# Kernel tuning notes

Measured on AMD Instinct MI355X. Metric: run time of the kernel, lower is better.

The kernel has to match this reference:

```python
import jax, jax.numpy as jnp
import numpy as np

N_NODES = 50000
N_EDGES = 800000
IN_CH = 128
OUT_CH = 64


def setup_inputs() -> dict:
    key = jax.random.key(0)
    ks = jax.random.split(key, 8)
    cat = IN_CH + OUT_CH
    scale = 1.0 / np.sqrt(cat)
    return {
        "x": jax.random.normal(ks[0], (N_NODES, IN_CH), dtype=jnp.float32),
        "edge_index": jax.random.randint(ks[1], (2, N_EDGES), 0, N_NODES, dtype=jnp.int64),
        "edge_weight": jax.random.uniform(ks[2], (N_EDGES,), dtype=jnp.float32),
        "hidden_state": jax.random.normal(ks[3], (N_NODES, OUT_CH), dtype=jnp.float32),
        "W_z": jax.random.normal(ks[4], (cat, OUT_CH), dtype=jnp.float32) * scale,
        "b_z": jnp.zeros((OUT_CH,), dtype=jnp.float32),
        "W_r": jax.random.normal(ks[5], (cat, OUT_CH), dtype=jnp.float32) * scale,
        "b_r": jnp.zeros((OUT_CH,), dtype=jnp.float32),
        "W_h": jax.random.normal(ks[6], (cat, OUT_CH), dtype=jnp.float32) * scale,
        "b_h": jnp.zeros((OUT_CH,), dtype=jnp.float32),
    }


def _gcn_norm(row, col, w, num_nodes):
    # PyG GCNConv normalization with self-loops (fill_value=1):
    # norm_e = deg[row]^-1/2 * w_e * deg[col]^-1/2 over loop-augmented edges
    loops = jnp.arange(num_nodes, dtype=row.dtype)
    row = jnp.concatenate([row, loops])
    col = jnp.concatenate([col, loops])
    w = jnp.concatenate([w, jnp.ones((num_nodes,), dtype=w.dtype)])
    deg = jax.ops.segment_sum(w, col, num_segments=num_nodes)
    dinv = jnp.where(deg > 0, jax.lax.rsqrt(deg), 0.0)
    norm = dinv[row] * w * dinv[col]
    return row, col, norm


def _gcn_conv(x_cat, W, b, row, col, norm, num_nodes):
    h = x_cat @ W                                   # (N, out)
    msg = h[row] * norm[:, None]                    # (E+N, out) gather + scale
    out = jax.ops.segment_sum(msg, col, num_segments=num_nodes)
    return out + b


def reference(x, edge_index, edge_weight, hidden_state,
              W_z, b_z, W_r, b_r, W_h, b_h):
    n = x.shape[0]
    row, col, norm = _gcn_norm(edge_index[0], edge_index[1], edge_weight, n)
    xh = jnp.concatenate([x, hidden_state], axis=1)
    z = jax.nn.sigmoid(_gcn_conv(xh, W_z, b_z, row, col, norm, n))
    r = jax.nn.sigmoid(_gcn_conv(xh, W_r, b_r, row, col, norm, n))
    xrh = jnp.concatenate([x, r * hidden_state], axis=1)
    h_cand = jnp.tanh(_gcn_conv(xrh, W_h, b_h, row, col, norm, n))
    return z * hidden_state + (1.0 - z) * h_cand
```

## Files before the change

### kernel.cpp

```cpp
#include <hip/hip_runtime.h>
#include <hip/hip_bf16.h>
#include <cstdint>
#include <cstddef>

#define IN_CH   128
#define OUT_CH  64
#define CAT_CH  192

typedef short bf16x8 __attribute__((ext_vector_type(8)));
typedef float f32x4  __attribute__((ext_vector_type(4)));
typedef float f32x2  __attribute__((ext_vector_type(2)));
typedef unsigned long long u64;
typedef unsigned int u32;

__device__ __forceinline__ float sigmoidf_(float x) { return 1.f / (1.f + __expf(-x)); }

__device__ __forceinline__ unsigned short f2bf(float f) {
    u32 u = __float_as_uint(f);
    u32 r = (u + 0x7fffu + ((u >> 16) & 1u)) >> 16;
    return (unsigned short)r;
}
__device__ __forceinline__ float bflo(u32 v) { return __uint_as_float(v << 16); }
__device__ __forceinline__ float bfhi(u32 v) { return __uint_as_float(v & 0xffff0000u); }

__device__ __forceinline__ unsigned char f2e4m3(float f) {
    u32 p = __builtin_amdgcn_cvt_pk_fp8_f32(f, f, 0, false);
    return (unsigned char)p;
}
template <bool HI>
__device__ __forceinline__ f32x2 fp8pk(u32 v) {
    return __builtin_amdgcn_cvt_pk_f32_fp8((int)v, HI);
}

__global__ void detect_kernel(const unsigned int* __restrict__ ei, int* __restrict__ flag) {
    unsigned int v = ei[(threadIdx.x << 1) + 1];
    unsigned long long b = __ballot(v != 0u);
    if (threadIdx.x == 0) *flag = (b != 0ull) ? 1 : 0;
}

__device__ __forceinline__ int load_col(const void* ei, int i, int E, int f) {
    return f ? ((const int*)ei)[E + i] : (int)((const long long*)ei)[E + i];
}
__device__ __forceinline__ int load_row(const void* ei, int i, int E, int f) {
    return f ? ((const int*)ei)[i] : (int)((const long long*)ei)[i];
}

__global__ void hist2_kernel(const void* __restrict__ ei, const float* __restrict__ w,
                             u64* __restrict__ packed, u32* __restrict__ rank,
                             const int* __restrict__ flag, int E) {
    int i0 = (blockIdx.x * blockDim.x + threadIdx.x) * 4;
    if (i0 >= E) return;
    int f = *flag;
    u32 rk[4];
#pragma unroll
    for (int k = 0; k < 4; k++) {
        int i = i0 + k;
        if (i < E) {
            int c = load_col(ei, i, E, f);
            u32 wq = __float2uint_rn(w[i] * 1048576.0f);
            u64 old = atomicAdd(&packed[c], (1ull << 32) | (u64)wq);
            rk[k] = (u32)(old >> 32);
        }
    }
#pragma unroll
    for (int k = 0; k < 4; k++)
        if (i0 + k < E) rank[i0 + k] = rk[k];
}

__global__ __launch_bounds__(256) void scan1_kernel(const u64* __restrict__ packed,
                                                    float* __restrict__ dinv,
                                                    int* __restrict__ starts,
                                                    int* __restrict__ bsum, int n) {
    __shared__ int s[256];
    int i = blockIdx.x * 256 + threadIdx.x;
    int v = 0;
    if (i < n) {
        u64 p = packed[i];
        float wsum = (float)(u32)(p & 0xffffffffull) * (1.0f / 1048576.0f);
        dinv[i] = rsqrtf(1.0f + wsum);
        v = (int)(p >> 32);
    }
    s[threadIdx.x] = v;
    __syncthreads();
#pragma unroll
    for (int d = 1; d < 256; d <<= 1) {
        int t = (threadIdx.x >= d) ? s[threadIdx.x - d] : 0;
        __syncthreads();
        s[threadIdx.x] += t;
        __syncthreads();
    }
    if (i < n) starts[i] = s[threadIdx.x] - v;
    if (threadIdx.x == 255) bsum[blockIdx.x] = s[255];
}

__global__ __launch_bounds__(256) void scan2_kernel(int* __restrict__ bsum, int nb) {
    __shared__ int s[256];
    int t = threadIdx.x;
    int v = (t < nb) ? bsum[t] : 0;
    s[t] = v;
    __syncthreads();
#pragma unroll
    for (int d = 1; d < 256; d <<= 1) {
        int u = (t >= d) ? s[t - d] : 0;
        __syncthreads();
        s[t] += u;
        __syncthreads();
    }
    if (t < nb) bsum[t] = s[t] - v;
}

__global__ void scan3_kernel(int* __restrict__ starts, const int* __restrict__ boff,
                             int n, int E) {
    int i = blockIdx.x * blockDim.x + threadIdx.x;
    if (i == 0) starts[n] = E;
    if (i < n) starts[i] += boff[blockIdx.x];
}

__global__ void scatter2_kernel(const void* __restrict__ ei, const float* __restrict__ w,
                                const float* __restrict__ dinv, const int* __restrict__ starts,
                                const u32* __restrict__ rank, u64* __restrict__ pairs,
                                const int* __restrict__ flag, int E) {
    int i0 = (blockIdx.x * blockDim.x + threadIdx.x) * 4;
    if (i0 >= E) return;
    int f = *flag;
    int r[4], c[4];
#pragma unroll
    for (int k = 0; k < 4; k++) {
        int i = i0 + k;
        if (i < E) { r[k] = load_row(ei, i, E, f); c[k] = load_col(ei, i, E, f); }
    }
#pragma unroll
    for (int k = 0; k < 4; k++) {
        int i = i0 + k;
        if (i < E) {
            float nm = dinv[r[k]] * w[i] * dinv[c[k]];
            int pos = starts[c[k]] + (int)rank[i];
            pairs[pos] = ((u64)__float_as_uint(nm) << 32) | (u32)(r[k] << 7);
        }
    }
}

__global__ void cvt_kernel(const float* __restrict__ x, const float* __restrict__ hidden,
                           unsigned short* __restrict__ xb, unsigned short* __restrict__ hb,
                           int nx, int nh) {
    int i4 = (blockIdx.x * blockDim.x + threadIdx.x) * 4;
    if (i4 < nx) {
        float4 v = *(const float4*)&x[i4];
        ushort4 o = { f2bf(v.x), f2bf(v.y), f2bf(v.z), f2bf(v.w) };
        *(ushort4*)&xb[i4] = o;
    } else {
        int j = i4 - nx;
        if (j < nh) {
            float4 v = *(const float4*)&hidden[j];
            ushort4 o = { f2bf(v.x), f2bf(v.y), f2bf(v.z), f2bf(v.w) };
            *(ushort4*)&hb[j] = o;
        }
    }
}

__global__ void packW_kernel(const float* __restrict__ Wz, const float* __restrict__ Wr,
                             const float* __restrict__ Wh,
                             unsigned short* __restrict__ Bzrt, unsigned short* __restrict__ Wht) {
    int i = blockIdx.x * blockDim.x + threadIdx.x;
    if (i >= 192 * CAT_CH) return;
    int col = i / CAT_CH, k = i % CAT_CH;
    if (col < 128) {
        float v = (col < 64) ? Wz[k * 64 + col] : Wr[k * 64 + (col - 64)];
        Bzrt[col * CAT_CH + k] = f2bf(v);
    } else {
        Wht[(col - 128) * CAT_CH + k] = f2bf(Wh[k * 64 + (col - 128)]);
    }
}

template <int TN, bool FP8OUT>
__global__ __launch_bounds__(256) void gemm_bf16_kernel(
    const unsigned short* __restrict__ A0, int a0w,
    const unsigned short* __restrict__ A1, int a1w,
    const unsigned short* __restrict__ Bt,
    void* __restrict__ Cout, int nrows)
{
    __shared__ unsigned short As[128][48];
    __shared__ unsigned short Bs[TN][200];

    const int t = threadIdx.x, lane = t & 63, wave = t >> 6;
    const int rowBase = blockIdx.x * 128;

    for (int idx = t * 8; idx < TN * CAT_CH; idx += 256 * 8) {
        int col = idx / CAT_CH, k = idx % CAT_CH;
        *(int4*)&Bs[col][k] = *(const int4*)&Bt[idx];
    }

    f32x4 acc[2][TN / 16];
#pragma unroll
    for (int rf = 0; rf < 2; rf++)
#pragma unroll
        for (int cf = 0; cf < TN / 16; cf++) acc[rf][cf] = (f32x4){0.f, 0.f, 0.f, 0.f};

    const int srow = t >> 1, half = t & 1;
    int arow = rowBase + srow;
    if (arow >= nrows) arow = nrows - 1;

    for (int k0 = 0; k0 < CAT_CH; k0 += 32) {
        __syncthreads();
        {
            const unsigned short* src = (k0 < a0w)
                ? A0 + (size_t)arow * a0w + k0
                : A1 + (size_t)arow * a1w + (k0 - a0w);
            *(int4*)&As[srow][half * 16] = *(const int4*)(src + half * 16);
            *(int4*)&As[srow][half * 16 + 8] = *(const int4*)(src + half * 16 + 8);
        }
        __syncthreads();

        const int rbase = wave * 32;
        const int koff = (lane >> 4) * 8;
        bf16x8 a0 = *(const bf16x8*)&As[rbase + (lane & 15)][koff];
        bf16x8 a1 = *(const bf16x8*)&As[rbase + 16 + (lane & 15)][koff];
#pragma unroll
        for (int cf = 0; cf < TN / 16; cf++) {
            bf16x8 b = *(const bf16x8*)&Bs[cf * 16 + (lane & 15)][k0 + koff];
            acc[0][cf] = __builtin_amdgcn_mfma_f32_16x16x32_bf16(a0, b, acc[0][cf], 0, 0, 0);
            acc[1][cf] = __builtin_amdgcn_mfma_f32_16x16x32_bf16(a1, b, acc[1][cf], 0, 0, 0);
        }
    }

#pragma unroll
    for (int rf = 0; rf < 2; rf++)
#pragma unroll
        for (int cf = 0; cf < TN / 16; cf++) {
            int row0 = rowBase + wave * 32 + rf * 16 + (lane >> 4) * 4;
            int col  = cf * 16 + (lane & 15);
#pragma unroll
            for (int r = 0; r < 4; r++) {
                int row = row0 + r;
                if (row < nrows) {
                    if (FP8OUT)
                        ((unsigned char*)Cout)[(size_t)row * TN + col] = f2e4m3(acc[rf][cf][r]);
                    else
                        ((unsigned short*)Cout)[(size_t)row * TN + col] = f2bf(acc[rf][cf][r]);
                }
            }
        }
}

__global__ __launch_bounds__(256) void spmm_zr_kernel(
    const unsigned char* __restrict__ H8, const u64* __restrict__ pairs,
    const int* __restrict__ starts, const float* __restrict__ dinv,
    const float* __restrict__ hidden, const float* __restrict__ bz,
    const float* __restrict__ br, float* __restrict__ Z,
    unsigned short* __restrict__ RHb, int N)
{
    int node = (blockIdx.x * 256 + threadIdx.x) >> 6;
    if (node >= N) return;
    const int lane = threadIdx.x & 63;
    const int sub = lane & 31, half = lane >> 5;
    int s = starts[node], e = starts[node + 1];
    float d = dinv[node], d2 = d * d;

    float a0 = 0.f, a1 = 0.f, a2 = 0.f, a3 = 0.f;
    if (half == 0) {
        u32 sv = *(const u32*)&H8[(size_t)node * 128 + sub * 4];
        f32x2 s01 = fp8pk<false>(sv), s23 = fp8pk<true>(sv);
        a0 = s01.x * d2; a1 = s01.y * d2; a2 = s23.x * d2; a3 = s23.y * d2;
    }

    int j = s;
    int full = s + ((e - s) & ~15);
    for (; j < full; j += 16) {
        u32 hv[8]; float nm[8];
#pragma unroll
        for (int k = 0; k < 8; k++) {
            u64 p = pairs[j + k * 2 + half];
            nm[k] = __uint_as_float((u32)(p >> 32));
            hv[k] = *(const u32*)&H8[(size_t)(u32)p + sub * 4];
        }
#pragma unroll
        for (int k = 0; k < 8; k++) {
            f32x2 h01 = fp8pk<false>(hv[k]), h23 = fp8pk<true>(hv[k]);
            a0 = fmaf(h01.x, nm[k], a0); a1 = fmaf(h01.y, nm[k], a1);
            a2 = fmaf(h23.x, nm[k], a2); a3 = fmaf(h23.y, nm[k], a3);
        }
    }
    if (j < e) {
        u32 hv[8]; float nm[8];
#pragma unroll
        for (int k = 0; k < 8; k++) {
            int jj = j + k * 2 + half;
            u64 p = pairs[(jj < e) ? jj : (e - 1)];
            nm[k] = (jj < e) ? __uint_as_float((u32)(p >> 32)) : 0.f;
            hv[k] = *(const u32*)&H8[(size_t)(u32)p + sub * 4];
        }
#pragma unroll
        for (int k = 0; k < 8; k++) {
            f32x2 h01 = fp8pk<false>(hv[k]), h23 = fp8pk<true>(hv[k]);
            a0 = fmaf(h01.x, nm[k], a0); a1 = fmaf(h01.y, nm[k], a1);
            a2 = fmaf(h23.x, nm[k], a2); a3 = fmaf(h23.y, nm[k], a3);
        }
    }

    a0 += __shfl_xor(a0, 32, 64);
    a1 += __shfl_xor(a1, 32, 64);
    a2 += __shfl_xor(a2, 32, 64);
    a3 += __shfl_xor(a3, 32, 64);

    if (half == 0) {
        if (sub < 16) {
            int c = sub * 4;
            float4 b4 = *(const float4*)&bz[c];
            float4 o = { sigmoidf_(a0 + b4.x), sigmoidf_(a1 + b4.y),
                         sigmoidf_(a2 + b4.z), sigmoidf_(a3 + b4.w) };
            *(float4*)&Z[(size_t)node * 64 + c] = o;
        } else {
            int c = (sub - 16) * 4;
            float4 b4 = *(const float4*)&br[c];
            float4 hid = *(const float4*)&hidden[(size_t)node * 64 + c];
            float r0 = sigmoidf_(a0 + b4.x) * hid.x;
            float r1 = sigmoidf_(a1 + b4.y) * hid.y;
            float r2 = sigmoidf_(a2 + b4.z) * hid.z;
            float r3 = sigmoidf_(a3 + b4.w) * hid.w;
            ushort4 o = { f2bf(r0), f2bf(r1), f2bf(r2), f2bf(r3) };
            *(ushort4*)&RHb[(size_t)node * 64 + c] = o;
        }
    }
}

__global__ __launch_bounds__(256) void spmm_h_kernel(
    const unsigned short* __restrict__ H, const u64* __restrict__ pairs,
    const int* __restrict__ starts, const float* __restrict__ dinv,
    const float* __restrict__ hidden, const float* __restrict__ bh,
    const float* __restrict__ Z, float* __restrict__ out, int N)
{
    int node = (blockIdx.x * 256 + threadIdx.x) >> 6;
    if (node >= N) return;
    const int lane = threadIdx.x & 63;
    const int sub = lane & 31, half = lane >> 5;
    const unsigned char* Hb = (const unsigned char*)H;
    int s = starts[node], e = starts[node + 1];
    float d = dinv[node], d2 = d * d;

    float ax = 0.f, ay = 0.f;
    if (half == 0) {
        u32 sv = *(const u32*)&Hb[(size_t)node * 128 + sub * 4];
        ax = bflo(sv) * d2; ay = bfhi(sv) * d2;
    }

    int j = s;
    int full = s + ((e - s) & ~15);
    for (; j < full; j += 16) {
        u32 hv[8]; float nm[8];
#pragma unroll
        for (int k = 0; k < 8; k++) {
            u64 p = pairs[j + k * 2 + half];
            nm[k] = __uint_as_float((u32)(p >> 32));
            hv[k] = *(const u32*)&Hb[(size_t)(u32)p + sub * 4];
        }
#pragma unroll
        for (int k = 0; k < 8; k++) {
            ax = fmaf(bflo(hv[k]), nm[k], ax);
            ay = fmaf(bfhi(hv[k]), nm[k], ay);
        }
    }
    if (j < e) {
        u32 hv[8]; float nm[8];
#pragma unroll
        for (int k = 0; k < 8; k++) {
            int jj = j + k * 2 + half;
            u64 p = pairs[(jj < e) ? jj : (e - 1)];
            nm[k] = (jj < e) ? __uint_as_float((u32)(p >> 32)) : 0.f;
            hv[k] = *(const u32*)&Hb[(size_t)(u32)p + sub * 4];
        }
#pragma unroll
        for (int k = 0; k < 8; k++) {
            ax = fmaf(bflo(hv[k]), nm[k], ax);
            ay = fmaf(bfhi(hv[k]), nm[k], ay);
        }
    }

    ax += __shfl_xor(ax, 32, 64);
    ay += __shfl_xor(ay, 32, 64);

    if (half == 0) {
        int c = sub * 2;
        size_t idx = (size_t)node * 64 + c;
        float2 hid = *(const float2*)&hidden[idx];
        float2 z   = *(const float2*)&Z[idx];
        float hc0 = tanhf(ax + bh[c]);
        float hc1 = tanhf(ay + bh[c + 1]);
        float2 o = { z.x * hid.x + (1.f - z.x) * hc0,
                     z.y * hid.y + (1.f - z.y) * hc1 };
        *(float2*)&out[idx] = o;
    }
}

extern "C" void kernel_launch(void* const* d_in, const int* in_sizes, int n_in,
                              void* d_out, int out_size, void* d_ws, size_t ws_size,
                              hipStream_t stream) {
    const float* x      = (const float*)d_in[0];
    const void*  eidx   = d_in[1];
    const float* ew     = (const float*)d_in[2];
    const float* hidden = (const float*)d_in[3];
    const float* Wz     = (const float*)d_in[4];
    const float* bz     = (const float*)d_in[5];
    const float* Wr     = (const float*)d_in[6];
    const float* br     = (const float*)d_in[7];
    const float* Wh     = (const float*)d_in[8];
    const float* bh     = (const float*)d_in[9];
    float* out = (float*)d_out;

    const int E = in_sizes[2];
    const int N = in_sizes[3] / OUT_CH;

    char* base = (char*)d_ws;
    size_t off = 0;
    auto carve = [&](size_t bytes) -> char* {
        char* p = base + off;
        off = (off + bytes + 255) & ~(size_t)255;
        return p;
    };
    u64*   packed = (u64*)  carve((size_t)N * 8);
    u32*   rank   = (u32*)  carve((size_t)E * 4);
    float* dinv   = (float*)carve((size_t)N * 4);
    int*   starts = (int*)  carve((size_t)(N + 1) * 4);
    int*   bsum   = (int*)  carve(256 * 4);
    u64*   pairs  = (u64*)  carve((size_t)E * 8);
    unsigned short* xb   = (unsigned short*)carve((size_t)N * 128 * 2);
    unsigned short* hb   = (unsigned short*)carve((size_t)N * 64 * 2);
    unsigned char*  Hzr8 = (unsigned char*)carve((size_t)N * 128);
    unsigned short* RHb  = (unsigned short*)carve((size_t)N * 64 * 2);
    unsigned short* Hhb  = (unsigned short*)carve((size_t)N * 64 * 2);
    float* Z = (float*)carve((size_t)N * 64 * 4);
    unsigned short* Bzrt = (unsigned short*)carve((size_t)128 * CAT_CH * 2);
    unsigned short* Wht  = (unsigned short*)carve((size_t)64 * CAT_CH * 2);
    int* flag = (int*)carve(4);
    if (off > ws_size) return;

    const int B256 = 256;
    const int gE4 = (E + 1023) / 1024;
    const int gN = (N + B256 - 1) / B256;
    const int gM = (N + 127) / 128;
    const int gW = (N + 3) / 4;

    hipLaunchKernelGGL(detect_kernel, dim3(1), dim3(64), 0, stream,
                       (const unsigned int*)eidx, flag);

    (void)hipMemsetAsync(packed, 0, (size_t)N * 8, stream);
    hipLaunchKernelGGL(hist2_kernel, dim3(gE4), dim3(B256), 0, stream,
                       eidx, ew, packed, rank, flag, E);

    hipLaunchKernelGGL(scan1_kernel, dim3(gN), dim3(B256), 0, stream,
                       packed, dinv, starts, bsum, N);
    hipLaunchKernelGGL(scan2_kernel, dim3(1), dim3(B256), 0, stream, bsum, gN);
    hipLaunchKernelGGL(scan3_kernel, dim3(gN), dim3(B256), 0, stream, starts, bsum, N, E);

    hipLaunchKernelGGL(scatter2_kernel, dim3(gE4), dim3(B256), 0, stream,
                       eidx, ew, dinv, starts, rank, pairs, flag, E);

    hipLaunchKernelGGL(cvt_kernel, dim3((N * CAT_CH / 4 + 255) / 256), dim3(B256), 0, stream,
                       x, hidden, xb, hb, N * 128, N * 64);
    hipLaunchKernelGGL(packW_kernel, dim3((192 * CAT_CH + 255) / 256), dim3(B256), 0, stream,
                       Wz, Wr, Wh, Bzrt, Wht);

    hipLaunchKernelGGL((gemm_bf16_kernel<128, true>), dim3(gM), dim3(B256), 0, stream,
                       xb, 128, hb, 64, Bzrt, (void*)Hzr8, N);

    hipLaunchKernelGGL(spmm_zr_kernel, dim3(gW), dim3(B256), 0, stream,
                       Hzr8, pairs, starts, dinv, hidden, bz, br, Z, RHb, N);

    hipLaunchKernelGGL((gemm_bf16_kernel<64, false>), dim3(gM), dim3(B256), 0, stream,
                       xb, 128, RHb, 64, Wht, (void*)Hhb, N);

    hipLaunchKernelGGL(spmm_h_kernel, dim3(gW), dim3(B256), 0, stream,
                       Hhb, pairs, starts, dinv, hidden, bh, Z, out, N);
}
```

Measured before the change: 178.7 us.

## Shard degree histogram atomics across eight copies to cut contention

The per-node packed count/weight histogram is replicated into 8 shards, selected by block index, so that concurrent 64-bit atomics spread over more addresses. The scan kernel sums the shards per node and writes per-shard offsets, and the scatter kernel adds the shard offset to the rank, which now carries the shard id in its top bits. The histogram kernel also processes 2 edges per thread instead of 4. This costs a larger memset, 8x more histogram reads in the scan, and an extra gathered offset read per edge in the scatter.

```diff
diff --git a/kernel.cpp b/kernel.cpp
--- a/kernel.cpp
+++ b/kernel.cpp
@@ -46,39 +46,49 @@
 }
 
 __global__ void hist2_kernel(const void* __restrict__ ei, const float* __restrict__ w,
-                             u64* __restrict__ packed, u32* __restrict__ rank,
-                             const int* __restrict__ flag, int E) {
-    int i0 = (blockIdx.x * blockDim.x + threadIdx.x) * 4;
+                             u64* __restrict__ packed8, u32* __restrict__ rank,
+                             const int* __restrict__ flag, int E, int N) {
+    int i0 = (blockIdx.x * blockDim.x + threadIdx.x) * 2;
     if (i0 >= E) return;
+    const u32 shard = blockIdx.x & 7;
+    u64* __restrict__ shp = packed8 + (size_t)shard * N;
     int f = *flag;
-    u32 rk[4];
-#pragma unroll
-    for (int k = 0; k < 4; k++) {
+    u32 rk[2];
+#pragma unroll
+    for (int k = 0; k < 2; k++) {
         int i = i0 + k;
         if (i < E) {
             int c = load_col(ei, i, E, f);
             u32 wq = __float2uint_rn(w[i] * 1048576.0f);
-            u64 old = atomicAdd(&packed[c], (1ull << 32) | (u64)wq);
-            rk[k] = (u32)(old >> 32);
-        }
-    }
-#pragma unroll
-    for (int k = 0; k < 4; k++)
+            u64 old = atomicAdd(&shp[c], (1ull << 32) | (u64)wq);
+            rk[k] = (shard << 28) | (u32)(old >> 32);
+        }
+    }
+#pragma unroll
+    for (int k = 0; k < 2; k++)
         if (i0 + k < E) rank[i0 + k] = rk[k];
 }
 
-__global__ __launch_bounds__(256) void scan1_kernel(const u64* __restrict__ packed,
+__global__ __launch_bounds__(256) void scan1_kernel(const u64* __restrict__ packed8,
                                                     float* __restrict__ dinv,
+                                                    u32* __restrict__ shoff,
                                                     int* __restrict__ starts,
                                                     int* __restrict__ bsum, int n) {
     __shared__ int s[256];
     int i = blockIdx.x * 256 + threadIdx.x;
     int v = 0;
     if (i < n) {
-        u64 p = packed[i];
-        float wsum = (float)(u32)(p & 0xffffffffull) * (1.0f / 1048576.0f);
-        dinv[i] = rsqrtf(1.0f + wsum);
-        v = (int)(p >> 32);
+        u32 run = 0, wsum = 0;
+#pragma unroll
+        for (int sh = 0; sh < 8; sh++) {
+            u64 p = packed8[(size_t)sh * n + i];
+            shoff[(size_t)sh * n + i] = run;
+            run  += (u32)(p >> 32);
+            wsum += (u32)p;
+        }
+        float ws = (float)wsum * (1.0f / 1048576.0f);
+        dinv[i] = rsqrtf(1.0f + ws);
+        v = (int)run;
     }
     s[threadIdx.x] = v;
     __syncthreads();
@@ -118,8 +128,9 @@
 
 __global__ void scatter2_kernel(const void* __restrict__ ei, const float* __restrict__ w,
                                 const float* __restrict__ dinv, const int* __restrict__ starts,
-                                const u32* __restrict__ rank, u64* __restrict__ pairs,
-                                const int* __restrict__ flag, int E) {
+                                const u32* __restrict__ shoff, const u32* __restrict__ rank,
+                                u64* __restrict__ pairs, const int* __restrict__ flag,
+                                int E, int N) {
     int i0 = (blockIdx.x * blockDim.x + threadIdx.x) * 4;
     if (i0 >= E) return;
     int f = *flag;
@@ -134,7 +145,9 @@
         int i = i0 + k;
         if (i < E) {
             float nm = dinv[r[k]] * w[i] * dinv[c[k]];
-            int pos = starts[c[k]] + (int)rank[i];
+            u32 rk = rank[i];
+            u32 sh = rk >> 28, rks = rk & 0x0fffffffu;
+            int pos = starts[c[k]] + (int)shoff[(size_t)sh * N + c[k]] + (int)rks;
             pairs[pos] = ((u64)__float_as_uint(nm) << 32) | (u32)(r[k] << 7);
         }
     }
@@ -416,12 +429,13 @@
         off = (off + bytes + 255) & ~(size_t)255;
         return p;
     };
-    u64*   packed = (u64*)  carve((size_t)N * 8);
-    u32*   rank   = (u32*)  carve((size_t)E * 4);
-    float* dinv   = (float*)carve((size_t)N * 4);
-    int*   starts = (int*)  carve((size_t)(N + 1) * 4);
-    int*   bsum   = (int*)  carve(256 * 4);
-    u64*   pairs  = (u64*)  carve((size_t)E * 8);
+    u64*   packed8 = (u64*) carve((size_t)N * 8 * 8);
+    u32*   shoff   = (u32*) carve((size_t)N * 8 * 4);
+    u32*   rank    = (u32*) carve((size_t)E * 4);
+    float* dinv    = (float*)carve((size_t)N * 4);
+    int*   starts  = (int*)  carve((size_t)(N + 1) * 4);
+    int*   bsum    = (int*)  carve(256 * 4);
+    u64*   pairs   = (u64*)  carve((size_t)E * 8);
     unsigned short* xb   = (unsigned short*)carve((size_t)N * 128 * 2);
     unsigned short* hb   = (unsigned short*)carve((size_t)N * 64 * 2);
     unsigned char*  Hzr8 = (unsigned char*)carve((size_t)N * 128);
@@ -434,6 +448,7 @@
     if (off > ws_size) return;
 
     const int B256 = 256;
+    const int gE2 = (E + 511) / 512;
     const int gE4 = (E + 1023) / 1024;
     const int gN = (N + B256 - 1) / B256;
     const int gM = (N + 127) / 128;
@@ -442,17 +457,17 @@
     hipLaunchKernelGGL(detect_kernel, dim3(1), dim3(64), 0, stream,
                        (const unsigned int*)eidx, flag);
 
-    (void)hipMemsetAsync(packed, 0, (size_t)N * 8, stream);
-    hipLaunchKernelGGL(hist2_kernel, dim3(gE4), dim3(B256), 0, stream,
-                       eidx, ew, packed, rank, flag, E);
+    (void)hipMemsetAsync(packed8, 0, (size_t)N * 8 * 8, stream);
+    hipLaunchKernelGGL(hist2_kernel, dim3(gE2), dim3(B256), 0, stream,
+                       eidx, ew, packed8, rank, flag, E, N);
 
     hipLaunchKernelGGL(scan1_kernel, dim3(gN), dim3(B256), 0, stream,
-                       packed, dinv, starts, bsum, N);
+                       packed8, dinv, shoff, starts, bsum, N);
     hipLaunchKernelGGL(scan2_kernel, dim3(1), dim3(B256), 0, stream, bsum, gN);
     hipLaunchKernelGGL(scan3_kernel, dim3(gN), dim3(B256), 0, stream, starts, bsum, N, E);
 
     hipLaunchKernelGGL(scatter2_kernel, dim3(gE4), dim3(B256), 0, stream,
-                       eidx, ew, dinv, starts, rank, pairs, flag, E);
+                       eidx, ew, dinv, starts, shoff, rank, pairs, flag, E, N);
 
     hipLaunchKernelGGL(cvt_kernel, dim3((N * CAT_CH / 4 + 255) / 256), dim3(B256), 0, stream,
                        x, hidden, xb, hb, N * 128, N * 64);
```

Measured after the change: 179.7 us. Within noise of the previous version (+0.6%).
